# Optimization experiments

Measured on AMD Instinct MI355X. Metric: run time of the kernel, lower is better.

## Reference

```python
import jax, jax.numpy as jnp
import numpy as np
from jax import lax


def setup_inputs() -> dict:
    key = jax.random.key(0)
    ks = jax.random.split(key, 12)
    B, T = 64, 256
    H, EN, ET, D = 512, 256, 256, 256  # hidden, embN, embT, embT_dyn (==ET since embedding_sizeT_dyn=None)
    VN, VT, VS = 300, 1000, 100       # vocab_sizeN, vocab_sizeT, num static ids (static_x_ids = range(100))
    s = 0.05
    ar = jnp.arange(VT)
    inp = {}
    inp["n_input"] = jax.random.randint(ks[0], (B, T), 0, VN)
    inp["t_input"] = jax.random.randint(ks[1], (B, T), 0, VT)
    inp["is_static_vocab"] = ar < VS                      # membership test (t in static_x_ids)
    inp["static2dense"] = jnp.where(ar < VS, ar, 0)       # static id -> row in embeddingT
    inp["dynamic2dense"] = jnp.where(ar >= VS, ar - VS, 0)  # dynamic id -> dense dynamic slot
    inp["embN"] = jax.random.normal(ks[2], (VN, EN)) * s
    inp["embT"] = jax.random.normal(ks[3], (VS, ET)) * s
    inp["W_ih"] = jax.random.normal(ks[4], (4 * H, EN + ET)) * s
    inp["W_hh"] = jax.random.normal(ks[5], (4 * H, H)) * s
    inp["b_ih"] = jax.random.normal(ks[6], (4 * H,)) * s
    inp["b_hh"] = jax.random.normal(ks[7], (4 * H,)) * s
    inp["Wd_ih"] = jax.random.normal(ks[8], (4 * D, EN + H)) * s
    inp["Wd_hh"] = jax.random.normal(ks[9], (4 * D, D)) * s
    inp["bd_ih"] = jax.random.normal(ks[10], (4 * D,)) * s
    inp["bd_hh"] = jax.random.normal(ks[11], (4 * D,)) * s
    inp["hid_init"] = jnp.zeros((H,))
    inp["cell_init"] = jnp.zeros((H,))
    inp["dyn_init_h"] = jnp.zeros((1, D))  # anonym_type='pure_zeros'
    inp["dyn_init_c"] = jnp.zeros((1, D))
    return inp


def _lstm_cell(x, h, c, Wi, Wh, bi, bh):
    # torch.nn.LSTMCell gate order: i, f, g, o
    g = x @ Wi.T + bi + h @ Wh.T + bh
    i, f, gg, o = jnp.split(g, 4, axis=-1)
    c2 = jax.nn.sigmoid(f) * c + jax.nn.sigmoid(i) * jnp.tanh(gg)
    return jax.nn.sigmoid(o) * jnp.tanh(c2), c2


def reference(n_input, t_input, is_static_vocab, static2dense, dynamic2dense,
              embN, embT, W_ih, W_hh, b_ih, b_hh,
              Wd_ih, Wd_hh, bd_ih, bd_hh,
              hid_init, cell_init, dyn_init_h, dyn_init_c):
    # The torch module's growing (lookup_table, de_h, de_c) cache is equivalent to
    # per-(batch, dynamic-token) state arrays Hd/Cd [B, V_dyn, D] with a 'seen' flag:
    # each (b, token) pair owns exactly one cache slot that is read/updated in place.
    B, T = n_input.shape
    H = hid_init.shape[0]
    D = dyn_init_h.shape[-1]
    VD = int(dynamic2dense.max()) + 1  # number of dynamic vocab slots (static at setup)
    bidx = jnp.arange(B)
    init_h = jnp.broadcast_to(dyn_init_h, (B, D))
    init_c = jnp.broadcast_to(dyn_init_c, (B, D))

    def step(carry, xt):
        h, c, seen, Hd, Cd = carry
        nt, tt = xt
        is_st = is_static_vocab[tt]            # [B] bool
        didx = dynamic2dense[tt]               # [B] dynamic slot (garbage 0 for static rows, masked below)
        sn = seen[bidx, didx]                  # was this (b, token) created before?
        hd_prev = jnp.where(sn[:, None], Hd[bidx, didx], init_h)
        cd_prev = jnp.where(sn[:, None], Cd[bidx, didx], init_c)
        n_emb = embN[nt]                       # [B, EN] (dropout=0 -> plain lookup)
        # emb_transform is identity (embedding_sizeT_dyn is None)
        h_tensor = jnp.where(is_st[:, None], embT[static2dense[tt]], hd_prev)  # [B, ET]
        h_new, c_new = _lstm_cell(jnp.concatenate([n_emb, h_tensor], 1), h, c, W_ih, W_hh, b_ih, b_hh)
        # dynamic-embedding LSTM: input is (n_emb, previous main hidden h)
        hd_new, cd_new = _lstm_cell(jnp.concatenate([n_emb, h], 1), hd_prev, cd_prev, Wd_ih, Wd_hh, bd_ih, bd_hh)
        dyn = (~is_st)[:, None]
        Hd = Hd.at[bidx, didx].set(jnp.where(dyn, hd_new, Hd[bidx, didx]))
        Cd = Cd.at[bidx, didx].set(jnp.where(dyn, cd_new, Cd[bidx, didx]))
        seen = seen.at[bidx, didx].set(sn | (~is_st))
        return (h_new, c_new, seen, Hd, Cd), h_new

    h0 = jnp.broadcast_to(hid_init, (B, H)) + 0.0
    c0 = jnp.broadcast_to(cell_init, (B, H)) + 0.0
    carry0 = (h0, c0,
              jnp.zeros((B, VD), dtype=bool),
              jnp.zeros((B, VD, D), dtype=embN.dtype),
              jnp.zeros((B, VD, D), dtype=embN.dtype))
    _, outs = lax.scan(step, carry0, (n_input.T, t_input.T))  # outs: [T, B, H]
    return jnp.transpose(outs, (1, 0, 2))                     # [B, T, H]
```

## Files before the change

### kernel.cpp

```cpp
#include <hip/hip_runtime.h>


typedef _Float16 f16;
typedef _Float16 f16x4 __attribute__((ext_vector_type(4)));
typedef _Float16 f16x8 __attribute__((ext_vector_type(8)));
typedef float f32x4 __attribute__((ext_vector_type(4)));

#define B_ 64
#define T_ 256
#define H_ 512
#define EN_ 256
#define ET_ 256
#define D_ 256
#define VN_ 300
#define VS_ 100

#define NB_MAIN_ 128
#define NB_DYN_ 64
#define NBLK_ 192
#define NTHR_ 256
#define NSH_ 64
#define PER_SHARD_ (NBLK_ / NSH_)
#define POLL_CAP_ (1u << 22)

static constexpr size_t OFF_CNT  = 0;
static constexpr size_t OFF_EMBN = 4096;
static constexpr size_t OFF_EMBT = OFF_EMBN + (size_t)VN_ * EN_ * 2;
static constexpr size_t OFF_DINH = OFF_EMBT + (size_t)VS_ * ET_ * 2;
static constexpr size_t OFF_PREV = OFF_DINH + 1024;
static constexpr size_t OFF_HH   = OFF_PREV + (size_t)T_ * B_ * 4;
static constexpr size_t OFF_HD   = OFF_HH + (size_t)(T_ + 1) * B_ * H_ * 2;
static constexpr size_t OFF_CD   = OFF_HD + (size_t)T_ * B_ * D_ * 2;
static constexpr size_t WS_NEED  = OFF_CD + (size_t)T_ * B_ * D_ * 4;

struct RnnParams {
  const int* n_input; const int* t_input; const int* s2d;
  const float* W_ih; const float* W_hh; const float* b_ih; const float* b_hh;
  const float* Wd_ih; const float* Wd_hh; const float* bd_ih; const float* bd_hh;
  const float* cell_init; const float* dyn_init_c;
  const f16* embN16; const f16* embT16; const f16* dynih16;
  const int* prev;
  f16* Hhist; f16* HdHist; float* CdHist;
  float* out; unsigned* cnt;
};

__device__ __forceinline__ float sigm(float x) { return 1.f / (1.f + __expf(-x)); }
__device__ __forceinline__ float tanh_fast(float x) {
  float e = __expf(2.f * x);
  return 1.f - 2.f / (e + 1.f);
}

__device__ __forceinline__ void cstore8(void* p, unsigned long long v) {
  __hip_atomic_store((unsigned long long*)p, v, __ATOMIC_RELAXED,
                     __HIP_MEMORY_SCOPE_AGENT);
}
__device__ __forceinline__ void cstore16(void* p, f32x4 v) {
  asm volatile("global_store_dwordx4 %0, %1, off sc0 sc1"
               :: "v"(p), "v"(v) : "memory");
}
__device__ __forceinline__ float4 scload16f(const float* p) {
  float4 v;
  asm volatile("global_load_dwordx4 %0, %1, off sc0 sc1\n\ts_waitcnt vmcnt(0)"
               : "=&v"(v) : "v"(p) : "memory");
  return v;
}
__device__ __forceinline__ void lds_barrier() {
  asm volatile("s_waitcnt lgkmcnt(0)\n\ts_barrier" ::: "memory");
}

__global__ void setup_kernel(const float* embN, const float* embT,
                             const float* hid_init, const float* dyn_init_h,
                             f16* embN16, f16* embT16, f16* dynih16,
                             f16* Hhist0, unsigned* cnt) {
  int i = blockIdx.x * blockDim.x + threadIdx.x;
  if (i < 1024)      cnt[i] = 0u;
  if (i < VN_ * EN_) embN16[i] = (f16)embN[i];
  if (i < VS_ * ET_) embT16[i] = (f16)embT[i];
  if (i < D_)        dynih16[i] = (f16)dyn_init_h[i];
  if (i < B_ * H_) {
    int b = i >> 9, k = i & 511;
    Hhist0[(k >> 2) * 256 + b * 4 + (k & 3)] = (f16)hid_init[k];
  }
  __threadfence();
}

__global__ void prev_kernel(const int* t_input, const int* s2d, int* prev) {
  int idx = blockIdx.x * blockDim.x + threadIdx.x;
  if (idx < B_ * T_) {
    int b = idx / T_, t = idx % T_;
    int tt = t_input[b * T_ + t];
    int p = -1;
    if (s2d[tt] != tt) {
      for (int q = t - 1; q >= 0; --q)
        if (t_input[b * T_ + q] == tt) { p = q; break; }
    }
    prev[t * B_ + b] = p;
  }
  __threadfence();
}

__device__ __forceinline__ void resolve(const RnnParams& p, bool isDyn, int t, int b,
                                        int tprev,
                                        const f16** aN, const f16** aX,
                                        const float** aC, int* dynw, int* rc) {
  const int nt = p.n_input[b * T_ + t];
  aN[b] = p.embN16 + (size_t)nt * EN_;
  const int tt = p.t_input[b * T_ + t];
  const int pv = p.prev[t * B_ + b];
  rc[b] = (pv >= 0 && pv == tprev) ? 1 : 0;
  const f16* hd = (pv >= 0) ? (p.HdHist + ((size_t)pv * B_ + b) * D_) : p.dynih16;
  const int s2 = p.s2d[tt];
  const bool st = (s2 == tt);
  if (!isDyn) {
    aX[b] = st ? (p.embT16 + (size_t)s2 * ET_) : hd;
  } else {
    aX[b] = hd;
    aC[b] = (pv >= 0) ? (p.CdHist + ((size_t)pv * B_ + b) * D_) : p.dyn_init_c;
    dynw[b] = st ? 0 : 1;
  }
}

__global__ __launch_bounds__(NTHR_, 1) void rnn_main(RnnParams p) {
  const int blk  = blockIdx.x;
  const int tid  = threadIdx.x;
  const int wave = tid >> 6;
  const int lane = tid & 63;
  const bool isDyn = (blk >= NB_MAIN_);
  const int u0 = isDyn ? (blk - NB_MAIN_) * 4 : blk * 4;

  __threadfence();

  __shared__ float s_bias[16];
  __shared__ float s_scr[64][17];
  __shared__ const f16*  s_aN[2][64];
  __shared__ const f16*  s_aX[2][64];
  __shared__ const float* s_aC[2][64];
  __shared__ int s_dynw[2][64];
  __shared__ int s_rc[2][64];

  const int nIdx = lane & 15;
  const int ui = nIdx & 3, gate = nIdx >> 2;
  const int ko = (lane >> 4) * 8;
  f16x8 w[32];
  if (!isDyn) {
    const int r = gate * H_ + u0 + ui;
#pragma unroll
    for (int s = 0; s < 32; ++s) {
      const int k = s * 32 + ko;
      const float* src = (k < 512) ? (p.W_ih + (size_t)r * 512 + k)
                                   : (p.W_hh + (size_t)r * 512 + (k - 512));
      f16x8 v;
#pragma unroll
      for (int j = 0; j < 8; ++j) v[j] = (f16)src[j];
      w[s] = v;
    }
  } else {
    const int r = gate * D_ + u0 + ui;
#pragma unroll
    for (int s = 0; s < 32; ++s) {
      const int k = s * 32 + ko;
      const float* src = (k < 768) ? (p.Wd_ih + (size_t)r * 768 + k)
                                   : (p.Wd_hh + (size_t)r * 256 + (k - 768));
      f16x8 v;
#pragma unroll
      for (int j = 0; j < 8; ++j) v[j] = (f16)src[j];
      w[s] = v;
    }
  }
  if (tid < 16) {
    int g2 = tid >> 2, un2 = tid & 3;
    s_bias[tid] = isDyn ? (p.bd_ih[g2 * D_ + u0 + un2] + p.bd_hh[g2 * D_ + u0 + un2])
                        : (p.b_ih[g2 * H_ + u0 + un2] + p.b_hh[g2 * H_ + u0 + un2]);
  }
  float creg[4] = {0.f, 0.f, 0.f, 0.f};
  if (tid < 64 && !isDyn) {
#pragma unroll
    for (int un = 0; un < 4; ++un) creg[un] = p.cell_init[u0 + un];
  }
  if (tid < 64)
    resolve(p, isDyn, 0, tid, -1, s_aN[0], s_aX[0], s_aC[0], s_dynw[0], s_rc[0]);
  __syncthreads();

  const int b = (wave << 4) + (lane & 15);
  f16x8 pf[16];
  float4 cvp = {0.f, 0.f, 0.f, 0.f};
  {
    const f16* pN = s_aN[0][b];
    const f16* pX = s_aX[0][b];
#pragma unroll
    for (int i = 0; i < 8; ++i) pf[i] = *(const f16x8*)(pN + i * 32 + ko);
#pragma unroll
    for (int i = 0; i < 8; ++i) pf[8 + i] = *(const f16x8*)(pX + i * 32 + ko);
    if (isDyn && tid < 64) cvp = *(const float4*)(s_aC[0][tid] + u0);
  }
  const int hoff = ((ko >> 2) << 8) + (b << 2);

  for (int t = 0; t < T_; ++t) {
    const int pb = t & 1;

    const f16* pH2 = p.Hhist + (size_t)t * 32768 + hoff;
    f16x8 hh[16];
#pragma unroll
    for (int i = 0; i < 16; ++i) {
      f16x4* h4 = (f16x4*)&hh[i];
      h4[0] = *(const f16x4*)(pH2 + i * 2048);
      h4[1] = *(const f16x4*)(pH2 + i * 2048 + 256);
    }

    {
      const int need = s_rc[pb][b];
      if (__any(need)) {
        if (need) {
          const f16* pX = s_aX[pb][b];
#pragma unroll
          for (int i = 0; i < 8; ++i)
            asm volatile("global_load_dwordx4 %0, %1, off sc0 sc1"
                         : "=&v"(pf[8 + i]) : "v"(pX + i * 32 + ko));
        }
        asm volatile("s_waitcnt vmcnt(0)" ::: "memory");
        __builtin_amdgcn_sched_barrier(0);
      }
    }

    f32x4 ac[4] = {{0,0,0,0},{0,0,0,0},{0,0,0,0},{0,0,0,0}};
    if (!isDyn) {
#pragma unroll
      for (int i = 0; i < 8; ++i)
        ac[i & 3] = __builtin_amdgcn_mfma_f32_16x16x32_f16(pf[i], w[i], ac[i & 3], 0, 0, 0);
#pragma unroll
      for (int i = 0; i < 8; ++i)
        ac[i & 3] = __builtin_amdgcn_mfma_f32_16x16x32_f16(pf[8 + i], w[8 + i], ac[i & 3], 0, 0, 0);
#pragma unroll
      for (int i = 0; i < 16; ++i)
        ac[i & 3] = __builtin_amdgcn_mfma_f32_16x16x32_f16(hh[i], w[16 + i], ac[i & 3], 0, 0, 0);
    } else {
#pragma unroll
      for (int i = 0; i < 8; ++i)
        ac[i & 3] = __builtin_amdgcn_mfma_f32_16x16x32_f16(pf[i], w[i], ac[i & 3], 0, 0, 0);
#pragma unroll
      for (int i = 0; i < 8; ++i)
        ac[i & 3] = __builtin_amdgcn_mfma_f32_16x16x32_f16(pf[8 + i], w[24 + i], ac[i & 3], 0, 0, 0);
#pragma unroll
      for (int i = 0; i < 16; ++i)
        ac[i & 3] = __builtin_amdgcn_mfma_f32_16x16x32_f16(hh[i], w[8 + i], ac[i & 3], 0, 0, 0);
    }
    f32x4 acc = (ac[0] + ac[1]) + (ac[2] + ac[3]);
#pragma unroll
    for (int j = 0; j < 4; ++j)
      s_scr[(wave << 4) + ((lane >> 4) << 2) + j][lane & 15] = acc[j];
    lds_barrier();

    float4 ho = {0.f, 0.f, 0.f, 0.f};
    if (tid < 64) {
      const int eb = tid;
      if (isDyn) {
        const int cneed = s_rc[pb][eb];
        if (__any(cneed)) {
          if (cneed) cvp = scload16f(s_aC[pb][eb] + u0);
          __builtin_amdgcn_sched_barrier(0);
        }
      }
      float g[16];
#pragma unroll
      for (int n = 0; n < 16; ++n) g[n] = s_scr[eb][n] + s_bias[n];
      if (!isDyn) {
        union { f16 h[4]; unsigned long long u; } pk;
#pragma unroll
        for (int un = 0; un < 4; ++un) {
          float c = sigm(g[4 + un]) * creg[un] + sigm(g[un]) * tanh_fast(g[8 + un]);
          creg[un] = c;
          float h = sigm(g[12 + un]) * tanh_fast(c);
          (&ho.x)[un] = h;
          pk.h[un] = (f16)h;
        }
        cstore8(&p.Hhist[(size_t)(t + 1) * 32768 + (size_t)(u0 >> 2) * 256
                         + (size_t)eb * 4], pk.u);
      } else {
        const float cold[4] = {cvp.x, cvp.y, cvp.z, cvp.w};
        f32x4 co;
        union { f16 h[4]; unsigned long long u; } pk;
#pragma unroll
        for (int un = 0; un < 4; ++un) {
          float c = sigm(g[4 + un]) * cold[un] + sigm(g[un]) * tanh_fast(g[8 + un]);
          float h = sigm(g[12 + un]) * tanh_fast(c);
          pk.h[un] = (f16)h;
          co[un] = c;
        }
        if (s_dynw[pb][eb]) {
          cstore8(&p.HdHist[((size_t)t * B_ + eb) * D_ + u0], pk.u);
          cstore16(&p.CdHist[((size_t)t * B_ + eb) * D_ + u0], co);
        }
      }
    } else if (tid < 128 && t + 1 < T_) {
      resolve(p, isDyn, t + 1, tid - 64, t,
              s_aN[pb ^ 1], s_aX[pb ^ 1], s_aC[pb ^ 1], s_dynw[pb ^ 1], s_rc[pb ^ 1]);
    }
    lds_barrier();

    if (t + 1 < T_) {
      if (wave == 0) {
        asm volatile("s_waitcnt vmcnt(0)" ::: "memory");
        if (tid == 0)
          __hip_atomic_fetch_add(&p.cnt[(blk & (NSH_ - 1)) << 4], 1u,
                                 __ATOMIC_RELAXED, __HIP_MEMORY_SCOPE_AGENT);
      }
      if (tid < 64 && !isDyn)
        *(float4*)&p.out[((size_t)tid * T_ + t) * H_ + u0] = ho;
      {
        const f16* pN2 = s_aN[pb ^ 1][b];
        const f16* pX2 = s_aX[pb ^ 1][b];
#pragma unroll
        for (int i = 0; i < 8; ++i) pf[i] = *(const f16x8*)(pN2 + i * 32 + ko);
#pragma unroll
        for (int i = 0; i < 8; ++i) pf[8 + i] = *(const f16x8*)(pX2 + i * 32 + ko);
        if (isDyn && tid < 64) cvp = *(const float4*)(s_aC[pb ^ 1][tid] + u0);
      }
      if (wave == 1) {
        const unsigned tgt = (unsigned)(t + 1) * PER_SHARD_;
        unsigned it = 0;
        while (__hip_atomic_load(&p.cnt[lane << 4], __ATOMIC_RELAXED,
                                 __HIP_MEMORY_SCOPE_AGENT) < tgt &&
               ++it < POLL_CAP_)
          __builtin_amdgcn_s_sleep(1);
      }
      lds_barrier();
    } else {
      if (tid < 64 && !isDyn)
        *(float4*)&p.out[((size_t)tid * T_ + t) * H_ + u0] = ho;
    }
  }
}

extern "C" void kernel_launch(void* const* d_in, const int* in_sizes, int n_in,
                              void* d_out, int out_size, void* d_ws, size_t ws_size,
                              hipStream_t stream) {
  (void)in_sizes; (void)n_in; (void)out_size;
  const int* n_input   = (const int*)d_in[0];
  const int* t_input   = (const int*)d_in[1];
  const int* s2d       = (const int*)d_in[3];
  const float* embN    = (const float*)d_in[5];
  const float* embT    = (const float*)d_in[6];
  const float* W_ih    = (const float*)d_in[7];
  const float* W_hh    = (const float*)d_in[8];
  const float* b_ih    = (const float*)d_in[9];
  const float* b_hh    = (const float*)d_in[10];
  const float* Wd_ih   = (const float*)d_in[11];
  const float* Wd_hh   = (const float*)d_in[12];
  const float* bd_ih   = (const float*)d_in[13];
  const float* bd_hh   = (const float*)d_in[14];
  const float* hid_init  = (const float*)d_in[15];
  const float* cell_init = (const float*)d_in[16];
  const float* dyn_init_h = (const float*)d_in[17];
  const float* dyn_init_c = (const float*)d_in[18];

  char* ws = (char*)d_ws;
  unsigned* cnt  = (unsigned*)(ws + OFF_CNT);
  f16* embN16    = (f16*)(ws + OFF_EMBN);
  f16* embT16    = (f16*)(ws + OFF_EMBT);
  f16* dynih16   = (f16*)(ws + OFF_DINH);
  int* prev      = (int*)(ws + OFF_PREV);
  f16* Hhist     = (f16*)(ws + OFF_HH);
  f16* HdHist    = (f16*)(ws + OFF_HD);
  float* CdHist  = (float*)(ws + OFF_CD);
  if (ws_size < WS_NEED) return;

  setup_kernel<<<dim3((VN_ * EN_ + NTHR_ - 1) / NTHR_), dim3(NTHR_), 0, stream>>>(
      embN, embT, hid_init, dyn_init_h, embN16, embT16, dynih16, Hhist, cnt);
  prev_kernel<<<dim3((B_ * T_ + NTHR_ - 1) / NTHR_), dim3(NTHR_), 0, stream>>>(
      t_input, s2d, prev);

  RnnParams prm;
  prm.n_input = n_input; prm.t_input = t_input; prm.s2d = s2d;
  prm.W_ih = W_ih; prm.W_hh = W_hh; prm.b_ih = b_ih; prm.b_hh = b_hh;
  prm.Wd_ih = Wd_ih; prm.Wd_hh = Wd_hh; prm.bd_ih = bd_ih; prm.bd_hh = bd_hh;
  prm.cell_init = cell_init; prm.dyn_init_c = dyn_init_c;
  prm.embN16 = embN16; prm.embT16 = embT16; prm.dynih16 = dynih16;
  prm.prev = prev; prm.Hhist = Hhist; prm.HdHist = HdHist; prm.CdHist = CdHist;
  prm.out = (float*)d_out; prm.cnt = cnt;

  void* args[] = { &prm };
  hipError_t e = hipLaunchCooperativeKernel((const void*)rnn_main,
                                            dim3(NBLK_), dim3(NTHR_), args, 0, stream);
  if (e != hipSuccess) {
    rnn_main<<<dim3(NBLK_), dim3(NTHR_), 0, stream>>>(prm);
  }
}
```

Baseline: 1.162 ms.

## Interleave dynamic h/c history in fp16 and defer output writes to kernel end

Replaces the separate fp16 Hd history and fp32 Cd history with one interleaved fp16 buffer. Each dynamic block writes one 16-byte packet of 4 h and 4 c values per batch row per step, without the dynw guard. Reads become strided 8-byte loads of h and c from the same line. Output writes are taken out of the recurrent loop and done at the end from the fp16 Hhist, which shortens each step's critical path but lowers output and cell-state precision to fp16.

Result: slower. 1.224 ms (+5.3%).

```diff
diff --git a/kernel.cpp b/kernel.cpp
--- a/kernel.cpp
+++ b/kernel.cpp
@@ -26,21 +26,20 @@
 static constexpr size_t OFF_CNT  = 0;
 static constexpr size_t OFF_EMBN = 4096;
 static constexpr size_t OFF_EMBT = OFF_EMBN + (size_t)VN_ * EN_ * 2;
-static constexpr size_t OFF_DINH = OFF_EMBT + (size_t)VS_ * ET_ * 2;
-static constexpr size_t OFF_PREV = OFF_DINH + 1024;
+static constexpr size_t OFF_DIT  = OFF_EMBT + (size_t)VS_ * ET_ * 2;
+static constexpr size_t OFF_PREV = OFF_DIT + 1024;
 static constexpr size_t OFF_HH   = OFF_PREV + (size_t)T_ * B_ * 4;
-static constexpr size_t OFF_HD   = OFF_HH + (size_t)(T_ + 1) * B_ * H_ * 2;
-static constexpr size_t OFF_CD   = OFF_HD + (size_t)T_ * B_ * D_ * 2;
-static constexpr size_t WS_NEED  = OFF_CD + (size_t)T_ * B_ * D_ * 4;
+static constexpr size_t OFF_DH   = OFF_HH + (size_t)(T_ + 1) * B_ * H_ * 2;
+static constexpr size_t WS_NEED  = OFF_DH + (size_t)T_ * 64 * 64 * 8 * 2;
 
 struct RnnParams {
   const int* n_input; const int* t_input; const int* s2d;
   const float* W_ih; const float* W_hh; const float* b_ih; const float* b_hh;
   const float* Wd_ih; const float* Wd_hh; const float* bd_ih; const float* bd_hh;
-  const float* cell_init; const float* dyn_init_c;
-  const f16* embN16; const f16* embT16; const f16* dynih16;
+  const float* cell_init;
+  const f16* embN16; const f16* embT16; const f16* dynT;
   const int* prev;
-  f16* Hhist; f16* HdHist; float* CdHist;
+  f16* Hhist; f16* DynHist;
   float* out; unsigned* cnt;
 };
 
@@ -54,13 +53,13 @@
   __hip_atomic_store((unsigned long long*)p, v, __ATOMIC_RELAXED,
                      __HIP_MEMORY_SCOPE_AGENT);
 }
-__device__ __forceinline__ void cstore16(void* p, f32x4 v) {
+__device__ __forceinline__ void cstore16h(void* p, f16x8 v) {
   asm volatile("global_store_dwordx4 %0, %1, off sc0 sc1"
                :: "v"(p), "v"(v) : "memory");
 }
-__device__ __forceinline__ float4 scload16f(const float* p) {
-  float4 v;
-  asm volatile("global_load_dwordx4 %0, %1, off sc0 sc1\n\ts_waitcnt vmcnt(0)"
+__device__ __forceinline__ f16x4 scload8h(const f16* p) {
+  f16x4 v;
+  asm volatile("global_load_dwordx2 %0, %1, off sc0 sc1\n\ts_waitcnt vmcnt(0)"
                : "=&v"(v) : "v"(p) : "memory");
   return v;
 }
@@ -70,13 +69,17 @@
 
 __global__ void setup_kernel(const float* embN, const float* embT,
                              const float* hid_init, const float* dyn_init_h,
-                             f16* embN16, f16* embT16, f16* dynih16,
+                             const float* dyn_init_c,
+                             f16* embN16, f16* embT16, f16* dynT,
                              f16* Hhist0, unsigned* cnt) {
   int i = blockIdx.x * blockDim.x + threadIdx.x;
   if (i < 1024)      cnt[i] = 0u;
   if (i < VN_ * EN_) embN16[i] = (f16)embN[i];
   if (i < VS_ * ET_) embT16[i] = (f16)embT[i];
-  if (i < D_)        dynih16[i] = (f16)dyn_init_h[i];
+  if (i < 512) {
+    int g = i >> 3, j = i & 7;
+    dynT[i] = (f16)((j < 4) ? dyn_init_h[g * 4 + j] : dyn_init_c[g * 4 + (j - 4)]);
+  }
   if (i < B_ * H_) {
     int b = i >> 9, k = i & 511;
     Hhist0[(k >> 2) * 256 + b * 4 + (k & 3)] = (f16)hid_init[k];
@@ -102,21 +105,22 @@
 __device__ __forceinline__ void resolve(const RnnParams& p, bool isDyn, int t, int b,
                                         int tprev,
                                         const f16** aN, const f16** aX,
-                                        const float** aC, int* dynw, int* rc) {
+                                        int* sx, int* rc) {
   const int nt = p.n_input[b * T_ + t];
   aN[b] = p.embN16 + (size_t)nt * EN_;
   const int tt = p.t_input[b * T_ + t];
   const int pv = p.prev[t * B_ + b];
   rc[b] = (pv >= 0 && pv == tprev) ? 1 : 0;
-  const f16* hd = (pv >= 0) ? (p.HdHist + ((size_t)pv * B_ + b) * D_) : p.dynih16;
   const int s2 = p.s2d[tt];
-  const bool st = (s2 == tt);
-  if (!isDyn) {
-    aX[b] = st ? (p.embT16 + (size_t)s2 * ET_) : hd;
+  if (!isDyn && s2 == tt) {
+    aX[b] = p.embT16 + (size_t)s2 * ET_;
+    sx[b] = 4;
+  } else if (pv >= 0) {
+    aX[b] = p.DynHist + (size_t)pv * 32768 + (size_t)b * 8;
+    sx[b] = 512;
   } else {
-    aX[b] = hd;
-    aC[b] = (pv >= 0) ? (p.CdHist + ((size_t)pv * B_ + b) * D_) : p.dyn_init_c;
-    dynw[b] = st ? 0 : 1;
+    aX[b] = p.dynT;
+    sx[b] = 8;
   }
 }
 
@@ -127,15 +131,15 @@
   const int lane = tid & 63;
   const bool isDyn = (blk >= NB_MAIN_);
   const int u0 = isDyn ? (blk - NB_MAIN_) * 4 : blk * 4;
+  const int gb = blk - NB_MAIN_;
 
   __threadfence();
 
   __shared__ float s_bias[16];
   __shared__ float s_scr[64][17];
-  __shared__ const f16*  s_aN[2][64];
-  __shared__ const f16*  s_aX[2][64];
-  __shared__ const float* s_aC[2][64];
-  __shared__ int s_dynw[2][64];
+  __shared__ const f16* s_aN[2][64];
+  __shared__ const f16* s_aX[2][64];
+  __shared__ int s_sx[2][64];
   __shared__ int s_rc[2][64];
 
   const int nIdx = lane & 15;
@@ -178,22 +182,31 @@
     for (int un = 0; un < 4; ++un) creg[un] = p.cell_init[u0 + un];
   }
   if (tid < 64)
-    resolve(p, isDyn, 0, tid, -1, s_aN[0], s_aX[0], s_aC[0], s_dynw[0], s_rc[0]);
+    resolve(p, isDyn, 0, tid, -1, s_aN[0], s_aX[0], s_sx[0], s_rc[0]);
   __syncthreads();
 
   const int b = (wave << 4) + (lane & 15);
+  const int gq = ko >> 2;
   f16x8 pf[16];
-  float4 cvp = {0.f, 0.f, 0.f, 0.f};
+  f16x4 cvq = {0, 0, 0, 0};
   {
     const f16* pN = s_aN[0][b];
-    const f16* pX = s_aX[0][b];
+    const f16* bX = s_aX[0][b];
+    const int sx = s_sx[0][b];
 #pragma unroll
     for (int i = 0; i < 8; ++i) pf[i] = *(const f16x8*)(pN + i * 32 + ko);
 #pragma unroll
-    for (int i = 0; i < 8; ++i) pf[8 + i] = *(const f16x8*)(pX + i * 32 + ko);
-    if (isDyn && tid < 64) cvp = *(const float4*)(s_aC[0][tid] + u0);
-  }
-  const int hoff = ((ko >> 2) << 8) + (b << 2);
+    for (int i = 0; i < 8; ++i) {
+      const int g0 = i * 8 + gq;
+      union { f16x4 q[2]; f16x8 o; } u;
+      u.q[0] = *(const f16x4*)(bX + (size_t)g0 * sx);
+      u.q[1] = *(const f16x4*)(bX + (size_t)(g0 + 1) * sx);
+      pf[8 + i] = u.o;
+    }
+    if (isDyn && tid < 64)
+      cvq = *(const f16x4*)(s_aX[0][tid] + 4 + (size_t)gb * s_sx[0][tid]);
+  }
+  const int hoff = (gq << 8) + (b << 2);
 
   for (int t = 0; t < T_; ++t) {
     const int pb = t & 1;
@@ -210,15 +223,29 @@
     {
       const int need = s_rc[pb][b];
       if (__any(need)) {
+        f16x4 lo[8], hi[8];
         if (need) {
-          const f16* pX = s_aX[pb][b];
-#pragma unroll
-          for (int i = 0; i < 8; ++i)
-            asm volatile("global_load_dwordx4 %0, %1, off sc0 sc1"
-                         : "=&v"(pf[8 + i]) : "v"(pX + i * 32 + ko));
+          const f16* bX = s_aX[pb][b];
+          const int sx = s_sx[pb][b];
+#pragma unroll
+          for (int i = 0; i < 8; ++i) {
+            const int g0 = i * 8 + gq;
+            asm volatile("global_load_dwordx2 %0, %1, off sc0 sc1"
+                         : "=&v"(lo[i]) : "v"(bX + (size_t)g0 * sx));
+            asm volatile("global_load_dwordx2 %0, %1, off sc0 sc1"
+                         : "=&v"(hi[i]) : "v"(bX + (size_t)(g0 + 1) * sx));
+          }
         }
         asm volatile("s_waitcnt vmcnt(0)" ::: "memory");
         __builtin_amdgcn_sched_barrier(0);
+        if (need) {
+#pragma unroll
+          for (int i = 0; i < 8; ++i) {
+            union { f16x4 q[2]; f16x8 o; } u;
+            u.q[0] = lo[i]; u.q[1] = hi[i];
+            pf[8 + i] = u.o;
+          }
+        }
       }
     }
 
@@ -250,13 +277,13 @@
       s_scr[(wave << 4) + ((lane >> 4) << 2) + j][lane & 15] = acc[j];
     lds_barrier();
 
-    float4 ho = {0.f, 0.f, 0.f, 0.f};
     if (tid < 64) {
       const int eb = tid;
       if (isDyn) {
         const int cneed = s_rc[pb][eb];
         if (__any(cneed)) {
-          if (cneed) cvp = scload16f(s_aC[pb][eb] + u0);
+          if (cneed)
+            cvq = scload8h(s_aX[pb][eb] + 4 + (size_t)gb * s_sx[pb][eb]);
           __builtin_amdgcn_sched_barrier(0);
         }
       }
@@ -270,30 +297,27 @@
           float c = sigm(g[4 + un]) * creg[un] + sigm(g[un]) * tanh_fast(g[8 + un]);
           creg[un] = c;
           float h = sigm(g[12 + un]) * tanh_fast(c);
-          (&ho.x)[un] = h;
           pk.h[un] = (f16)h;
         }
         cstore8(&p.Hhist[(size_t)(t + 1) * 32768 + (size_t)(u0 >> 2) * 256
                          + (size_t)eb * 4], pk.u);
       } else {
-        const float cold[4] = {cvp.x, cvp.y, cvp.z, cvp.w};
-        f32x4 co;
-        union { f16 h[4]; unsigned long long u; } pk;
+        const float cold[4] = {(float)cvq[0], (float)cvq[1],
+                               (float)cvq[2], (float)cvq[3]};
+        f16x8 pk;
 #pragma unroll
         for (int un = 0; un < 4; ++un) {
           float c = sigm(g[4 + un]) * cold[un] + sigm(g[un]) * tanh_fast(g[8 + un]);
           float h = sigm(g[12 + un]) * tanh_fast(c);
-          pk.h[un] = (f16)h;
-          co[un] = c;
-        }
-        if (s_dynw[pb][eb]) {
-          cstore8(&p.HdHist[((size_t)t * B_ + eb) * D_ + u0], pk.u);
-          cstore16(&p.CdHist[((size_t)t * B_ + eb) * D_ + u0], co);
-        }
+          pk[un] = (f16)h;
+          pk[4 + un] = (f16)c;
+        }
+        cstore16h(&p.DynHist[(size_t)t * 32768 + (size_t)gb * 512
+                             + (size_t)eb * 8], pk);
       }
     } else if (tid < 128 && t + 1 < T_) {
       resolve(p, isDyn, t + 1, tid - 64, t,
-              s_aN[pb ^ 1], s_aX[pb ^ 1], s_aC[pb ^ 1], s_dynw[pb ^ 1], s_rc[pb ^ 1]);
+              s_aN[pb ^ 1], s_aX[pb ^ 1], s_sx[pb ^ 1], s_rc[pb ^ 1]);
     }
     lds_barrier();
 
@@ -304,16 +328,23 @@
           __hip_atomic_fetch_add(&p.cnt[(blk & (NSH_ - 1)) << 4], 1u,
                                  __ATOMIC_RELAXED, __HIP_MEMORY_SCOPE_AGENT);
       }
-      if (tid < 64 && !isDyn)
-        *(float4*)&p.out[((size_t)tid * T_ + t) * H_ + u0] = ho;
       {
         const f16* pN2 = s_aN[pb ^ 1][b];
-        const f16* pX2 = s_aX[pb ^ 1][b];
+        const f16* bX2 = s_aX[pb ^ 1][b];
+        const int sx2 = s_sx[pb ^ 1][b];
 #pragma unroll
         for (int i = 0; i < 8; ++i) pf[i] = *(const f16x8*)(pN2 + i * 32 + ko);
 #pragma unroll
-        for (int i = 0; i < 8; ++i) pf[8 + i] = *(const f16x8*)(pX2 + i * 32 + ko);
-        if (isDyn && tid < 64) cvp = *(const float4*)(s_aC[pb ^ 1][tid] + u0);
+        for (int i = 0; i < 8; ++i) {
+          const int g0 = i * 8 + gq;
+          union { f16x4 q[2]; f16x8 o; } u;
+          u.q[0] = *(const f16x4*)(bX2 + (size_t)g0 * sx2);
+          u.q[1] = *(const f16x4*)(bX2 + (size_t)(g0 + 1) * sx2);
+          pf[8 + i] = u.o;
+        }
+        if (isDyn && tid < 64)
+          cvq = *(const f16x4*)(s_aX[pb ^ 1][tid] + 4
+                                + (size_t)gb * s_sx[pb ^ 1][tid]);
       }
       if (wave == 1) {
         const unsigned tgt = (unsigned)(t + 1) * PER_SHARD_;
@@ -324,9 +355,21 @@
           __builtin_amdgcn_s_sleep(1);
       }
       lds_barrier();
-    } else {
-      if (tid < 64 && !isDyn)
-        *(float4*)&p.out[((size_t)tid * T_ + t) * H_ + u0] = ho;
+    }
+  }
+
+  asm volatile("s_waitcnt vmcnt(0)" ::: "memory");
+  if (!isDyn) {
+    const int ob = tid & 63;
+    const int tq = tid >> 6;
+    const int gm = u0 >> 2;
+    for (int i = 0; i < 64; ++i) {
+      const int t = (tq << 6) + i;
+      f16x4 hv = *(const f16x4*)(p.Hhist + (size_t)(t + 1) * 32768
+                                 + (size_t)gm * 256 + (size_t)ob * 4);
+      float4 o;
+      o.x = (float)hv[0]; o.y = (float)hv[1]; o.z = (float)hv[2]; o.w = (float)hv[3];
+      *(float4*)&p.out[((size_t)ob * T_ + t) * H_ + u0] = o;
     }
   }
 }
@@ -357,15 +400,15 @@
   unsigned* cnt  = (unsigned*)(ws + OFF_CNT);
   f16* embN16    = (f16*)(ws + OFF_EMBN);
   f16* embT16    = (f16*)(ws + OFF_EMBT);
-  f16* dynih16   = (f16*)(ws + OFF_DINH);
+  f16* dynT      = (f16*)(ws + OFF_DIT);
   int* prev      = (int*)(ws + OFF_PREV);
   f16* Hhist     = (f16*)(ws + OFF_HH);
-  f16* HdHist    = (f16*)(ws + OFF_HD);
-  float* CdHist  = (float*)(ws + OFF_CD);
+  f16* DynHist   = (f16*)(ws + OFF_DH);
   if (ws_size < WS_NEED) return;
 
   setup_kernel<<<dim3((VN_ * EN_ + NTHR_ - 1) / NTHR_), dim3(NTHR_), 0, stream>>>(
-      embN, embT, hid_init, dyn_init_h, embN16, embT16, dynih16, Hhist, cnt);
+      embN, embT, hid_init, dyn_init_h, dyn_init_c,
+      embN16, embT16, dynT, Hhist, cnt);
   prev_kernel<<<dim3((B_ * T_ + NTHR_ - 1) / NTHR_), dim3(NTHR_), 0, stream>>>(
       t_input, s2d, prev);
 
@@ -373,9 +416,9 @@
   prm.n_input = n_input; prm.t_input = t_input; prm.s2d = s2d;
   prm.W_ih = W_ih; prm.W_hh = W_hh; prm.b_ih = b_ih; prm.b_hh = b_hh;
   prm.Wd_ih = Wd_ih; prm.Wd_hh = Wd_hh; prm.bd_ih = bd_ih; prm.bd_hh = bd_hh;
-  prm.cell_init = cell_init; prm.dyn_init_c = dyn_init_c;
-  prm.embN16 = embN16; prm.embT16 = embT16; prm.dynih16 = dynih16;
-  prm.prev = prev; prm.Hhist = Hhist; prm.HdHist = HdHist; prm.CdHist = CdHist;
+  prm.cell_init = cell_init;
+  prm.embN16 = embN16; prm.embT16 = embT16; prm.dynT = dynT;
+  prm.prev = prev; prm.Hhist = Hhist; prm.DynHist = DynHist;
   prm.out = (float*)d_out; prm.cnt = cnt;
 
   void* args[] = { &prm };
```

## Halve persistent block count, give each block eight hidden units

Applied to the files above, without the earlier changes.

Cuts the persistent grid from 192 to 96 blocks. Each block now computes eight hidden units (two 16-column MFMA tiles) instead of four, and the barrier shards drop from 64 to 32. The aim is cheaper per-step grid-wide synchronisation, with fewer participants and counters to poll, and reuse of each loaded input and h fragment across twice as many MFMAs. The cost is double the weight registers per thread (64 f16x8 vectors), which raises register pressure and risks spills, plus longer serial per-step compute in each block.

Measured after the change: 1.571 ms. +35.2%, slower.

```diff
diff --git a/kernel.cpp b/kernel.cpp
--- a/kernel.cpp
+++ b/kernel.cpp
@@ -15,11 +15,11 @@
 #define VN_ 300
 #define VS_ 100
 
-#define NB_MAIN_ 128
-#define NB_DYN_ 64
-#define NBLK_ 192
+#define NB_MAIN_ 64
+#define NB_DYN_ 32
+#define NBLK_ 96
 #define NTHR_ 256
-#define NSH_ 64
+#define NSH_ 32
 #define PER_SHARD_ (NBLK_ / NSH_)
 #define POLL_CAP_ (1u << 22)
 
@@ -58,11 +58,12 @@
   asm volatile("global_store_dwordx4 %0, %1, off sc0 sc1"
                :: "v"(p), "v"(v) : "memory");
 }
-__device__ __forceinline__ float4 scload16f(const float* p) {
-  float4 v;
-  asm volatile("global_load_dwordx4 %0, %1, off sc0 sc1\n\ts_waitcnt vmcnt(0)"
-               : "=&v"(v) : "v"(p) : "memory");
-  return v;
+__device__ __forceinline__ void scload16f2(const float* p0, const float* p1,
+                                           float4& v0, float4& v1) {
+  asm volatile("global_load_dwordx4 %0, %2, off sc0 sc1\n\t"
+               "global_load_dwordx4 %1, %3, off sc0 sc1\n\t"
+               "s_waitcnt vmcnt(0)"
+               : "=&v"(v0), "=&v"(v1) : "v"(p0), "v"(p1) : "memory");
 }
 __device__ __forceinline__ void lds_barrier() {
   asm volatile("s_waitcnt lgkmcnt(0)\n\ts_barrier" ::: "memory");
@@ -126,12 +127,12 @@
   const int wave = tid >> 6;
   const int lane = tid & 63;
   const bool isDyn = (blk >= NB_MAIN_);
-  const int u0 = isDyn ? (blk - NB_MAIN_) * 4 : blk * 4;
+  const int u0 = isDyn ? (blk - NB_MAIN_) * 8 : blk * 8;
 
   __threadfence();
 
-  __shared__ float s_bias[16];
-  __shared__ float s_scr[64][17];
+  __shared__ float s_bias[32];
+  __shared__ float s_scr[64][33];
   __shared__ const f16*  s_aN[2][64];
   __shared__ const f16*  s_aX[2][64];
   __shared__ const float* s_aC[2][64];
@@ -141,41 +142,49 @@
   const int nIdx = lane & 15;
   const int ui = nIdx & 3, gate = nIdx >> 2;
   const int ko = (lane >> 4) * 8;
-  f16x8 w[32];
+  f16x8 w0[32], w1[32];
   if (!isDyn) {
-    const int r = gate * H_ + u0 + ui;
+    const int r0 = gate * H_ + u0 + ui;
+    const int r1 = r0 + 4;
 #pragma unroll
     for (int s = 0; s < 32; ++s) {
       const int k = s * 32 + ko;
-      const float* src = (k < 512) ? (p.W_ih + (size_t)r * 512 + k)
-                                   : (p.W_hh + (size_t)r * 512 + (k - 512));
-      f16x8 v;
-#pragma unroll
-      for (int j = 0; j < 8; ++j) v[j] = (f16)src[j];
-      w[s] = v;
+      const float* s0 = (k < 512) ? (p.W_ih + (size_t)r0 * 512 + k)
+                                  : (p.W_hh + (size_t)r0 * 512 + (k - 512));
+      const float* s1 = (k < 512) ? (p.W_ih + (size_t)r1 * 512 + k)
+                                  : (p.W_hh + (size_t)r1 * 512 + (k - 512));
+      f16x8 v0, v1;
+#pragma unroll
+      for (int j = 0; j < 8; ++j) { v0[j] = (f16)s0[j]; v1[j] = (f16)s1[j]; }
+      w0[s] = v0; w1[s] = v1;
     }
   } else {
-    const int r = gate * D_ + u0 + ui;
+    const int r0 = gate * D_ + u0 + ui;
+    const int r1 = r0 + 4;
 #pragma unroll
     for (int s = 0; s < 32; ++s) {
       const int k = s * 32 + ko;
-      const float* src = (k < 768) ? (p.Wd_ih + (size_t)r * 768 + k)
-                                   : (p.Wd_hh + (size_t)r * 256 + (k - 768));
-      f16x8 v;
-#pragma unroll
-      for (int j = 0; j < 8; ++j) v[j] = (f16)src[j];
-      w[s] = v;
-    }
-  }
-  if (tid < 16) {
-    int g2 = tid >> 2, un2 = tid & 3;
-    s_bias[tid] = isDyn ? (p.bd_ih[g2 * D_ + u0 + un2] + p.bd_hh[g2 * D_ + u0 + un2])
-                        : (p.b_ih[g2 * H_ + u0 + un2] + p.b_hh[g2 * H_ + u0 + un2]);
-  }
-  float creg[4] = {0.f, 0.f, 0.f, 0.f};
+      const float* s0 = (k < 768) ? (p.Wd_ih + (size_t)r0 * 768 + k)
+                                  : (p.Wd_hh + (size_t)r0 * 256 + (k - 768));
+      const float* s1 = (k < 768) ? (p.Wd_ih + (size_t)r1 * 768 + k)
+                                  : (p.Wd_hh + (size_t)r1 * 256 + (k - 768));
+      f16x8 v0, v1;
+#pragma unroll
+      for (int j = 0; j < 8; ++j) { v0[j] = (f16)s0[j]; v1[j] = (f16)s1[j]; }
+      w0[s] = v0; w1[s] = v1;
+    }
+  }
+  if (tid < 32) {
+    const int t2 = tid >> 4, q = tid & 15;
+    const int g2 = q >> 2, un = t2 * 4 + (q & 3);
+    s_bias[tid] = isDyn
+        ? (p.bd_ih[g2 * D_ + u0 + un] + p.bd_hh[g2 * D_ + u0 + un])
+        : (p.b_ih[g2 * H_ + u0 + un] + p.b_hh[g2 * H_ + u0 + un]);
+  }
+  float creg[8] = {0, 0, 0, 0, 0, 0, 0, 0};
   if (tid < 64 && !isDyn) {
 #pragma unroll
-    for (int un = 0; un < 4; ++un) creg[un] = p.cell_init[u0 + un];
+    for (int un = 0; un < 8; ++un) creg[un] = p.cell_init[u0 + un];
   }
   if (tid < 64)
     resolve(p, isDyn, 0, tid, -1, s_aN[0], s_aX[0], s_aC[0], s_dynw[0], s_rc[0]);
@@ -183,7 +192,7 @@
 
   const int b = (wave << 4) + (lane & 15);
   f16x8 pf[16];
-  float4 cvp = {0.f, 0.f, 0.f, 0.f};
+  float4 cvp0 = {0, 0, 0, 0}, cvp1 = {0, 0, 0, 0};
   {
     const f16* pN = s_aN[0][b];
     const f16* pX = s_aX[0][b];
@@ -191,7 +200,10 @@
     for (int i = 0; i < 8; ++i) pf[i] = *(const f16x8*)(pN + i * 32 + ko);
 #pragma unroll
     for (int i = 0; i < 8; ++i) pf[8 + i] = *(const f16x8*)(pX + i * 32 + ko);
-    if (isDyn && tid < 64) cvp = *(const float4*)(s_aC[0][tid] + u0);
+    if (isDyn && tid < 64) {
+      cvp0 = *(const float4*)(s_aC[0][tid] + u0);
+      cvp1 = *(const float4*)(s_aC[0][tid] + u0 + 4);
+    }
   }
   const int hoff = ((ko >> 2) << 8) + (b << 2);
 
@@ -222,73 +234,102 @@
       }
     }
 
-    f32x4 ac[4] = {{0,0,0,0},{0,0,0,0},{0,0,0,0},{0,0,0,0}};
+    f32x4 a0[4] = {{0,0,0,0},{0,0,0,0},{0,0,0,0},{0,0,0,0}};
+    f32x4 a1[4] = {{0,0,0,0},{0,0,0,0},{0,0,0,0},{0,0,0,0}};
     if (!isDyn) {
 #pragma unroll
-      for (int i = 0; i < 8; ++i)
-        ac[i & 3] = __builtin_amdgcn_mfma_f32_16x16x32_f16(pf[i], w[i], ac[i & 3], 0, 0, 0);
-#pragma unroll
-      for (int i = 0; i < 8; ++i)
-        ac[i & 3] = __builtin_amdgcn_mfma_f32_16x16x32_f16(pf[8 + i], w[8 + i], ac[i & 3], 0, 0, 0);
-#pragma unroll
-      for (int i = 0; i < 16; ++i)
-        ac[i & 3] = __builtin_amdgcn_mfma_f32_16x16x32_f16(hh[i], w[16 + i], ac[i & 3], 0, 0, 0);
+      for (int i = 0; i < 8; ++i) {
+        a0[i & 3] = __builtin_amdgcn_mfma_f32_16x16x32_f16(pf[i], w0[i], a0[i & 3], 0, 0, 0);
+        a1[i & 3] = __builtin_amdgcn_mfma_f32_16x16x32_f16(pf[i], w1[i], a1[i & 3], 0, 0, 0);
+      }
+#pragma unroll
+      for (int i = 0; i < 8; ++i) {
+        a0[i & 3] = __builtin_amdgcn_mfma_f32_16x16x32_f16(pf[8 + i], w0[8 + i], a0[i & 3], 0, 0, 0);
+        a1[i & 3] = __builtin_amdgcn_mfma_f32_16x16x32_f16(pf[8 + i], w1[8 + i], a1[i & 3], 0, 0, 0);
+      }
+#pragma unroll
+      for (int i = 0; i < 16; ++i) {
+        a0[i & 3] = __builtin_amdgcn_mfma_f32_16x16x32_f16(hh[i], w0[16 + i], a0[i & 3], 0, 0, 0);
+        a1[i & 3] = __builtin_amdgcn_mfma_f32_16x16x32_f16(hh[i], w1[16 + i], a1[i & 3], 0, 0, 0);
+      }
     } else {
 #pragma unroll
-      for (int i = 0; i < 8; ++i)
-        ac[i & 3] = __builtin_amdgcn_mfma_f32_16x16x32_f16(pf[i], w[i], ac[i & 3], 0, 0, 0);
-#pragma unroll
-      for (int i = 0; i < 8; ++i)
-        ac[i & 3] = __builtin_amdgcn_mfma_f32_16x16x32_f16(pf[8 + i], w[24 + i], ac[i & 3], 0, 0, 0);
-#pragma unroll
-      for (int i = 0; i < 16; ++i)
-        ac[i & 3] = __builtin_amdgcn_mfma_f32_16x16x32_f16(hh[i], w[8 + i], ac[i & 3], 0, 0, 0);
-    }
-    f32x4 acc = (ac[0] + ac[1]) + (ac[2] + ac[3]);
-#pragma unroll
-    for (int j = 0; j < 4; ++j)
-      s_scr[(wave << 4) + ((lane >> 4) << 2) + j][lane & 15] = acc[j];
+      for (int i = 0; i < 8; ++i) {
+        a0[i & 3] = __builtin_amdgcn_mfma_f32_16x16x32_f16(pf[i], w0[i], a0[i & 3], 0, 0, 0);
+        a1[i & 3] = __builtin_amdgcn_mfma_f32_16x16x32_f16(pf[i], w1[i], a1[i & 3], 0, 0, 0);
+      }
+#pragma unroll
+      for (int i = 0; i < 8; ++i) {
+        a0[i & 3] = __builtin_amdgcn_mfma_f32_16x16x32_f16(pf[8 + i], w0[24 + i], a0[i & 3], 0, 0, 0);
+        a1[i & 3] = __builtin_amdgcn_mfma_f32_16x16x32_f16(pf[8 + i], w1[24 + i], a1[i & 3], 0, 0, 0);
+      }
+#pragma unroll
+      for (int i = 0; i < 16; ++i) {
+        a0[i & 3] = __builtin_amdgcn_mfma_f32_16x16x32_f16(hh[i], w0[8 + i], a0[i & 3], 0, 0, 0);
+        a1[i & 3] = __builtin_amdgcn_mfma_f32_16x16x32_f16(hh[i], w1[8 + i], a1[i & 3], 0, 0, 0);
+      }
+    }
+    f32x4 s0 = (a0[0] + a0[1]) + (a0[2] + a0[3]);
+    f32x4 s1 = (a1[0] + a1[1]) + (a1[2] + a1[3]);
+#pragma unroll
+    for (int j = 0; j < 4; ++j) {
+      const int row = (wave << 4) + ((lane >> 4) << 2) + j;
+      s_scr[row][lane & 15]      = s0[j];
+      s_scr[row][16 + (lane & 15)] = s1[j];
+    }
     lds_barrier();
 
-    float4 ho = {0.f, 0.f, 0.f, 0.f};
+    float4 ho0 = {0, 0, 0, 0}, ho1 = {0, 0, 0, 0};
     if (tid < 64) {
       const int eb = tid;
       if (isDyn) {
         const int cneed = s_rc[pb][eb];
         if (__any(cneed)) {
-          if (cneed) cvp = scload16f(s_aC[pb][eb] + u0);
+          if (cneed)
+            scload16f2(s_aC[pb][eb] + u0, s_aC[pb][eb] + u0 + 4, cvp0, cvp1);
           __builtin_amdgcn_sched_barrier(0);
         }
       }
-      float g[16];
-#pragma unroll
-      for (int n = 0; n < 16; ++n) g[n] = s_scr[eb][n] + s_bias[n];
+      float g[32];
+#pragma unroll
+      for (int n = 0; n < 32; ++n) g[n] = s_scr[eb][n] + s_bias[n];
       if (!isDyn) {
-        union { f16 h[4]; unsigned long long u; } pk;
-#pragma unroll
-        for (int un = 0; un < 4; ++un) {
-          float c = sigm(g[4 + un]) * creg[un] + sigm(g[un]) * tanh_fast(g[8 + un]);
-          creg[un] = c;
-          float h = sigm(g[12 + un]) * tanh_fast(c);
-          (&ho.x)[un] = h;
-          pk.h[un] = (f16)h;
+#pragma unroll
+        for (int h2 = 0; h2 < 2; ++h2) {
+          union { f16 h[4]; unsigned long long u; } pk;
+#pragma unroll
+          for (int un = 0; un < 4; ++un) {
+            const int base = h2 * 16;
+            float c = sigm(g[base + 4 + un]) * creg[h2 * 4 + un]
+                    + sigm(g[base + un]) * tanh_fast(g[base + 8 + un]);
+            creg[h2 * 4 + un] = c;
+            float h = sigm(g[base + 12 + un]) * tanh_fast(c);
+            (h2 ? (&ho1.x) : (&ho0.x))[un] = h;
+            pk.h[un] = (f16)h;
+          }
+          cstore8(&p.Hhist[(size_t)(t + 1) * 32768
+                           + (size_t)((u0 >> 2) + h2) * 256 + (size_t)eb * 4],
+                  pk.u);
         }
-        cstore8(&p.Hhist[(size_t)(t + 1) * 32768 + (size_t)(u0 >> 2) * 256
-                         + (size_t)eb * 4], pk.u);
       } else {
-        const float cold[4] = {cvp.x, cvp.y, cvp.z, cvp.w};
-        f32x4 co;
-        union { f16 h[4]; unsigned long long u; } pk;
-#pragma unroll
-        for (int un = 0; un < 4; ++un) {
-          float c = sigm(g[4 + un]) * cold[un] + sigm(g[un]) * tanh_fast(g[8 + un]);
-          float h = sigm(g[12 + un]) * tanh_fast(c);
-          pk.h[un] = (f16)h;
-          co[un] = c;
-        }
-        if (s_dynw[pb][eb]) {
-          cstore8(&p.HdHist[((size_t)t * B_ + eb) * D_ + u0], pk.u);
-          cstore16(&p.CdHist[((size_t)t * B_ + eb) * D_ + u0], co);
+        const float4 cvs[2] = {cvp0, cvp1};
+#pragma unroll
+        for (int h2 = 0; h2 < 2; ++h2) {
+          f32x4 co;
+          union { f16 h[4]; unsigned long long u; } pk;
+#pragma unroll
+          for (int un = 0; un < 4; ++un) {
+            const int base = h2 * 16;
+            float c = sigm(g[base + 4 + un]) * (&cvs[h2].x)[un]
+                    + sigm(g[base + un]) * tanh_fast(g[base + 8 + un]);
+            float h = sigm(g[base + 12 + un]) * tanh_fast(c);
+            pk.h[un] = (f16)h;
+            co[un] = c;
+          }
+          if (s_dynw[pb][eb]) {
+            cstore8(&p.HdHist[((size_t)t * B_ + eb) * D_ + u0 + h2 * 4], pk.u);
+            cstore16(&p.CdHist[((size_t)t * B_ + eb) * D_ + u0 + h2 * 4], co);
+          }
         }
       }
     } else if (tid < 128 && t + 1 < T_) {
@@ -304,8 +345,10 @@
           __hip_atomic_fetch_add(&p.cnt[(blk & (NSH_ - 1)) << 4], 1u,
                                  __ATOMIC_RELAXED, __HIP_MEMORY_SCOPE_AGENT);
       }
-      if (tid < 64 && !isDyn)
-        *(float4*)&p.out[((size_t)tid * T_ + t) * H_ + u0] = ho;
+      if (tid < 64 && !isDyn) {
+        *(float4*)&p.out[((size_t)tid * T_ + t) * H_ + u0] = ho0;
+        *(float4*)&p.out[((size_t)tid * T_ + t) * H_ + u0 + 4] = ho1;
+      }
       {
         const f16* pN2 = s_aN[pb ^ 1][b];
         const f16* pX2 = s_aX[pb ^ 1][b];
@@ -313,20 +356,25 @@
         for (int i = 0; i < 8; ++i) pf[i] = *(const f16x8*)(pN2 + i * 32 + ko);
 #pragma unroll
         for (int i = 0; i < 8; ++i) pf[8 + i] = *(const f16x8*)(pX2 + i * 32 + ko);
-        if (isDyn && tid < 64) cvp = *(const float4*)(s_aC[pb ^ 1][tid] + u0);
+        if (isDyn && tid < 64) {
+          cvp0 = *(const float4*)(s_aC[pb ^ 1][tid] + u0);
+          cvp1 = *(const float4*)(s_aC[pb ^ 1][tid] + u0 + 4);
+        }
       }
       if (wave == 1) {
         const unsigned tgt = (unsigned)(t + 1) * PER_SHARD_;
         unsigned it = 0;
-        while (__hip_atomic_load(&p.cnt[lane << 4], __ATOMIC_RELAXED,
+        while (__hip_atomic_load(&p.cnt[(lane & 31) << 4], __ATOMIC_RELAXED,
                                  __HIP_MEMORY_SCOPE_AGENT) < tgt &&
                ++it < POLL_CAP_)
           __builtin_amdgcn_s_sleep(1);
       }
       lds_barrier();
     } else {
-      if (tid < 64 && !isDyn)
-        *(float4*)&p.out[((size_t)tid * T_ + t) * H_ + u0] = ho;
+      if (tid < 64 && !isDyn) {
+        *(float4*)&p.out[((size_t)tid * T_ + t) * H_ + u0] = ho0;
+        *(float4*)&p.out[((size_t)tid * T_ + t) * H_ + u0 + 4] = ho1;
+      }
     }
   }
 }
```

## Precompute input-projection MFMAs before the grid barrier and retile CdHist layout

Applied to the files above, without the earlier changes.

Moves the MFMA products for the embedding and x-input operands of the next step ahead of the cross-block spin-wait, so only the recurrent h-history MFMAs remain on the critical path after the barrier. When the x operand must be reloaded because it came from the immediately previous step, its partial sum is recomputed. The CdHist cell-state history is re-laid out per 4-unit block so each block's reads and writes are contiguous across batch rows. This adds extra accumulator registers, may raise register pressure, and duplicates work on reload steps.

Result: no change. 1.174 ms (+1.0%).

```diff
diff --git a/kernel.cpp b/kernel.cpp
--- a/kernel.cpp
+++ b/kernel.cpp
@@ -31,7 +31,7 @@
 static constexpr size_t OFF_HH   = OFF_PREV + (size_t)T_ * B_ * 4;
 static constexpr size_t OFF_HD   = OFF_HH + (size_t)(T_ + 1) * B_ * H_ * 2;
 static constexpr size_t OFF_CD   = OFF_HD + (size_t)T_ * B_ * D_ * 2;
-static constexpr size_t WS_NEED  = OFF_CD + (size_t)T_ * B_ * D_ * 4;
+static constexpr size_t WS_NEED  = OFF_CD + (size_t)T_ * 64 * 64 * 4 * 4;
 
 struct RnnParams {
   const int* n_input; const int* t_input; const int* s2d;
@@ -100,7 +100,7 @@
 }
 
 __device__ __forceinline__ void resolve(const RnnParams& p, bool isDyn, int t, int b,
-                                        int tprev,
+                                        int tprev, int u0,
                                         const f16** aN, const f16** aX,
                                         const float** aC, int* dynw, int* rc) {
   const int nt = p.n_input[b * T_ + t];
@@ -115,7 +115,9 @@
     aX[b] = st ? (p.embT16 + (size_t)s2 * ET_) : hd;
   } else {
     aX[b] = hd;
-    aC[b] = (pv >= 0) ? (p.CdHist + ((size_t)pv * B_ + b) * D_) : p.dyn_init_c;
+    aC[b] = (pv >= 0)
+        ? (p.CdHist + (size_t)pv * 16384 + (size_t)(u0 >> 2) * 256 + (size_t)b * 4)
+        : (p.dyn_init_c + u0);
     dynw[b] = st ? 0 : 1;
   }
 }
@@ -178,12 +180,14 @@
     for (int un = 0; un < 4; ++un) creg[un] = p.cell_init[u0 + un];
   }
   if (tid < 64)
-    resolve(p, isDyn, 0, tid, -1, s_aN[0], s_aX[0], s_aC[0], s_dynw[0], s_rc[0]);
+    resolve(p, isDyn, 0, tid, -1, u0, s_aN[0], s_aX[0], s_aC[0], s_dynw[0], s_rc[0]);
   __syncthreads();
 
   const int b = (wave << 4) + (lane & 15);
   f16x8 pf[16];
   float4 cvp = {0.f, 0.f, 0.f, 0.f};
+  f32x4 acN[4] = {{0,0,0,0},{0,0,0,0},{0,0,0,0},{0,0,0,0}};
+  f32x4 acX[4] = {{0,0,0,0},{0,0,0,0},{0,0,0,0},{0,0,0,0}};
   {
     const f16* pN = s_aN[0][b];
     const f16* pX = s_aX[0][b];
@@ -191,7 +195,15 @@
     for (int i = 0; i < 8; ++i) pf[i] = *(const f16x8*)(pN + i * 32 + ko);
 #pragma unroll
     for (int i = 0; i < 8; ++i) pf[8 + i] = *(const f16x8*)(pX + i * 32 + ko);
-    if (isDyn && tid < 64) cvp = *(const float4*)(s_aC[0][tid] + u0);
+    if (isDyn && tid < 64) cvp = *(const float4*)(s_aC[0][tid]);
+#pragma unroll
+    for (int i = 0; i < 8; ++i)
+      acN[i & 3] = __builtin_amdgcn_mfma_f32_16x16x32_f16(pf[i], w[i], acN[i & 3], 0, 0, 0);
+#pragma unroll
+    for (int i = 0; i < 8; ++i) {
+      const int wi = isDyn ? (24 + i) : (8 + i);
+      acX[i & 3] = __builtin_amdgcn_mfma_f32_16x16x32_f16(pf[8 + i], w[wi], acX[i & 3], 0, 0, 0);
+    }
   }
   const int hoff = ((ko >> 2) << 8) + (b << 2);
 
@@ -219,32 +231,27 @@
         }
         asm volatile("s_waitcnt vmcnt(0)" ::: "memory");
         __builtin_amdgcn_sched_barrier(0);
-      }
-    }
-
-    f32x4 ac[4] = {{0,0,0,0},{0,0,0,0},{0,0,0,0},{0,0,0,0}};
+#pragma unroll
+        for (int i = 0; i < 4; ++i) acX[i] = (f32x4){0, 0, 0, 0};
+#pragma unroll
+        for (int i = 0; i < 8; ++i) {
+          const int wi = isDyn ? (24 + i) : (8 + i);
+          acX[i & 3] = __builtin_amdgcn_mfma_f32_16x16x32_f16(pf[8 + i], w[wi], acX[i & 3], 0, 0, 0);
+        }
+      }
+    }
+
     if (!isDyn) {
 #pragma unroll
-      for (int i = 0; i < 8; ++i)
-        ac[i & 3] = __builtin_amdgcn_mfma_f32_16x16x32_f16(pf[i], w[i], ac[i & 3], 0, 0, 0);
-#pragma unroll
-      for (int i = 0; i < 8; ++i)
-        ac[i & 3] = __builtin_amdgcn_mfma_f32_16x16x32_f16(pf[8 + i], w[8 + i], ac[i & 3], 0, 0, 0);
-#pragma unroll
       for (int i = 0; i < 16; ++i)
-        ac[i & 3] = __builtin_amdgcn_mfma_f32_16x16x32_f16(hh[i], w[16 + i], ac[i & 3], 0, 0, 0);
+        acN[i & 3] = __builtin_amdgcn_mfma_f32_16x16x32_f16(hh[i], w[16 + i], acN[i & 3], 0, 0, 0);
     } else {
 #pragma unroll
-      for (int i = 0; i < 8; ++i)
-        ac[i & 3] = __builtin_amdgcn_mfma_f32_16x16x32_f16(pf[i], w[i], ac[i & 3], 0, 0, 0);
-#pragma unroll
-      for (int i = 0; i < 8; ++i)
-        ac[i & 3] = __builtin_amdgcn_mfma_f32_16x16x32_f16(pf[8 + i], w[24 + i], ac[i & 3], 0, 0, 0);
-#pragma unroll
       for (int i = 0; i < 16; ++i)
-        ac[i & 3] = __builtin_amdgcn_mfma_f32_16x16x32_f16(hh[i], w[8 + i], ac[i & 3], 0, 0, 0);
-    }
-    f32x4 acc = (ac[0] + ac[1]) + (ac[2] + ac[3]);
+        acN[i & 3] = __builtin_amdgcn_mfma_f32_16x16x32_f16(hh[i], w[8 + i], acN[i & 3], 0, 0, 0);
+    }
+    f32x4 acc = ((acN[0] + acN[1]) + (acN[2] + acN[3]))
+              + ((acX[0] + acX[1]) + (acX[2] + acX[3]));
 #pragma unroll
     for (int j = 0; j < 4; ++j)
       s_scr[(wave << 4) + ((lane >> 4) << 2) + j][lane & 15] = acc[j];
@@ -256,7 +263,7 @@
       if (isDyn) {
         const int cneed = s_rc[pb][eb];
         if (__any(cneed)) {
-          if (cneed) cvp = scload16f(s_aC[pb][eb] + u0);
+          if (cneed) cvp = scload16f(s_aC[pb][eb]);
           __builtin_amdgcn_sched_barrier(0);
         }
       }
@@ -288,11 +295,12 @@
         }
         if (s_dynw[pb][eb]) {
           cstore8(&p.HdHist[((size_t)t * B_ + eb) * D_ + u0], pk.u);
-          cstore16(&p.CdHist[((size_t)t * B_ + eb) * D_ + u0], co);
+          cstore16(&p.CdHist[(size_t)t * 16384 + (size_t)(u0 >> 2) * 256
+                             + (size_t)eb * 4], co);
         }
       }
     } else if (tid < 128 && t + 1 < T_) {
-      resolve(p, isDyn, t + 1, tid - 64, t,
+      resolve(p, isDyn, t + 1, tid - 64, t, u0,
               s_aN[pb ^ 1], s_aX[pb ^ 1], s_aC[pb ^ 1], s_dynw[pb ^ 1], s_rc[pb ^ 1]);
     }
     lds_barrier();
@@ -313,7 +321,20 @@
         for (int i = 0; i < 8; ++i) pf[i] = *(const f16x8*)(pN2 + i * 32 + ko);
 #pragma unroll
         for (int i = 0; i < 8; ++i) pf[8 + i] = *(const f16x8*)(pX2 + i * 32 + ko);
-        if (isDyn && tid < 64) cvp = *(const float4*)(s_aC[pb ^ 1][tid] + u0);
+        if (isDyn && tid < 64) cvp = *(const float4*)(s_aC[pb ^ 1][tid]);
+#pragma unroll
+        for (int i = 0; i < 4; ++i) {
+          acN[i] = (f32x4){0, 0, 0, 0};
+          acX[i] = (f32x4){0, 0, 0, 0};
+        }
+#pragma unroll
+        for (int i = 0; i < 8; ++i)
+          acN[i & 3] = __builtin_amdgcn_mfma_f32_16x16x32_f16(pf[i], w[i], acN[i & 3], 0, 0, 0);
+#pragma unroll
+        for (int i = 0; i < 8; ++i) {
+          const int wi = isDyn ? (24 + i) : (8 + i);
+          acX[i & 3] = __builtin_amdgcn_mfma_f32_16x16x32_f16(pf[8 + i], w[wi], acX[i & 3], 0, 0, 0);
+        }
       }
       if (wave == 1) {
         const unsigned tgt = (unsigned)(t + 1) * PER_SHARD_;
```
